# Kernel optimization log

Measured on AMD Instinct MI355X. Metric: run time of the kernel, lower is better.

Reference implementation:

```python
import jax, jax.numpy as jnp
import numpy as np

B, S, H, D, R = 2, 2048, 16, 128, 16
HID = H * D
ROPE_BASE = 10000.0


def _rotate_half(x):
    x1, x2 = x[..., : D // 2], x[..., D // 2:]
    return jnp.concatenate((-x2, x1), axis=-1)


def _sin_cos(position_ids):
    # full-dim RoPE (rope_fraction == 1)
    inv_freq = 1.0 / (ROPE_BASE ** (jnp.arange(0, D, 2, dtype=jnp.float32) / D))  # [D/2]
    freqs = position_ids.astype(jnp.float32)[..., None] * inv_freq  # [B,S,D/2]
    emb = jnp.concatenate((freqs, freqs), axis=-1)  # [B,S,D]
    # add head axis -> [B,1,S,D]
    return jnp.sin(emb)[:, None], jnp.cos(emb)[:, None]


def setup_inputs() -> dict:
    key = jax.random.key(0)
    ks = jax.random.split(key, 6)
    q = jax.random.normal(ks[0], (B, S, HID), dtype=jnp.float32)
    k = jax.random.normal(ks[1], (B, S, HID), dtype=jnp.float32)
    v = jax.random.normal(ks[2], (B, S, HID), dtype=jnp.float32)
    position_ids = jnp.tile(jnp.arange(S, dtype=jnp.int64)[None], (B, 1))
    causal = jnp.tril(jnp.ones((S, S), dtype=bool))
    attention_mask = jnp.where(causal, 0.0, -1e9).astype(jnp.float32)
    attention_mask = jnp.broadcast_to(attention_mask[None, None], (B, 1, S, S))
    k_registers = jax.random.normal(ks[3], (1, H, R, D), dtype=jnp.float32)
    v_registers = jax.random.normal(ks[4], (1, H, R, D), dtype=jnp.float32)
    return {
        "query_states": q,
        "key_states": k,
        "value_states": v,
        "position_ids": position_ids,
        "attention_mask": attention_mask,
        "k_registers": k_registers,
        "v_registers": v_registers,
    }


def reference(query_states, key_states, value_states, position_ids,
              attention_mask, k_registers, v_registers):
    bsz, q_len, _ = query_states.shape
    # [B,S,H*D] -> [B,H,S,D]
    q = query_states.reshape(bsz, q_len, H, D).transpose(0, 2, 1, 3)
    k = key_states.reshape(bsz, -1, H, D).transpose(0, 2, 1, 3)
    v = value_states.reshape(bsz, -1, H, D).transpose(0, 2, 1, 3)

    sin, cos = _sin_cos(position_ids)
    q = q * cos + _rotate_half(q) * sin
    k = k * cos + _rotate_half(k) * sin

    # concat learned register K/V tokens along kv-length
    k = jnp.concatenate((k, jnp.broadcast_to(k_registers, (bsz, H, R, D))), axis=2)
    v = jnp.concatenate((v, jnp.broadcast_to(v_registers, (bsz, H, R, D))), axis=2)
    mask = jnp.concatenate(
        (attention_mask,
         jnp.zeros(attention_mask.shape[:-1] + (R,), dtype=attention_mask.dtype)),
        axis=-1)

    scale = 1.0 / np.sqrt(D).astype(np.float32)
    scores = jnp.einsum('bhqd,bhkd->bhqk', q, k * scale) + mask  # [B,H,S,S+R]
    probs = jax.nn.softmax(scores.astype(jnp.float32), axis=-1).astype(q.dtype)
    out = jnp.einsum('bhqk,bhkd->bhqd', probs, v)
    return out.transpose(0, 2, 1, 3).reshape(bsz, q_len, H * D)
```

## Files before the change

kernel.cpp:

```cpp
#include <hip/hip_runtime.h>

#define S_LEN 2048
#define HID   2048
#define NH    16
#define HD    128
#define NREG  16
#define KPAD  2112
#define NBH   32

typedef float f32x4 __attribute__((ext_vector_type(4)));
typedef short s16x8 __attribute__((ext_vector_type(8)));

__device__ __forceinline__ unsigned short f2bf(float f) {
    union { float f; unsigned int u; } x; x.f = f;
    return (unsigned short)((x.u + 0x7FFFu + ((x.u >> 16) & 1u)) >> 16);
}
__device__ __forceinline__ unsigned short f2bf_t(float f) {
    union { float f; unsigned int u; } x; x.f = f;
    return (unsigned short)(x.u >> 16);
}
__device__ __forceinline__ void gl_lds16(const unsigned short* g, unsigned short* l) {
    __builtin_amdgcn_global_load_lds((const __attribute__((address_space(1))) void*)g,
                                     (__attribute__((address_space(3))) void*)l, 16, 0, 0);
}

__global__ void rope_qk_kernel(const float* __restrict__ q, const float* __restrict__ k,
                               const int* __restrict__ pos,
                               unsigned short* __restrict__ Qb, unsigned short* __restrict__ Kb) {
    int i = blockIdx.x * 256 + threadIdx.x;
    int dh = i & 63;
    int h  = (i >> 6) & 15;
    int s  = (i >> 10) & 2047;
    int b  = i >> 21;
    float p   = (float)pos[b * S_LEN + s];
    float inv = exp2f((float)dh * -0.20762050593046014f);
    float ang = p * inv;
    float rev = ang * 0.15915494309189535f;
    rev -= rintf(rev);
    float a2 = rev * 6.283185307179586f;
    float sn = __sinf(a2), cs = __cosf(a2);
    const float* qp = q + (size_t)(b * S_LEN + s) * HID + h * HD + dh;
    const float* kp = k + (size_t)(b * S_LEN + s) * HID + h * HD + dh;
    float q1 = qp[0], q2 = qp[64];
    float k1 = kp[0], k2 = kp[64];
    const float scale = 0.08838834764831845f;
    size_t qo = (size_t)((b * NH + h) * S_LEN + s) * HD + dh;
    Qb[qo]      = f2bf((q1 * cs - q2 * sn) * scale);
    Qb[qo + 64] = f2bf((q2 * cs + q1 * sn) * scale);
    size_t ko = (size_t)((b * NH + h) * KPAD + s) * HD + dh;
    Kb[ko]      = f2bf(k1 * cs - k2 * sn);
    Kb[ko + 64] = f2bf(k2 * cs + k1 * sn);
}

__global__ void fill_regs_kernel(const float* __restrict__ kreg, const float* __restrict__ vreg,
                                 unsigned short* __restrict__ Kb, unsigned short* __restrict__ Vt) {
    int i = blockIdx.x * 256 + threadIdx.x;
    {
        int d = i & 127, r = (i >> 7) & 63, h = (i >> 13) & 15, b = i >> 17;
        float v = (r < NREG) ? kreg[(h * NREG + r) * HD + d] : 0.0f;
        Kb[((size_t)((b * NH + h) * KPAD + 2048 + r)) * HD + d] = f2bf(v);
    }
    {
        int r = i & 63, d = (i >> 6) & 127, h = (i >> 13) & 15, b = i >> 17;
        float v = (r < NREG) ? vreg[(h * NREG + r) * HD + d] : 0.0f;
        Vt[((size_t)((b * NH + h) * HD + d)) * KPAD + 2048 + r] = f2bf(v);
    }
}

__global__ void transpose_v_kernel(const float* __restrict__ v, unsigned short* __restrict__ Vt) {
    __shared__ unsigned short T[64][136];
    int t  = threadIdx.x;
    int bh = blockIdx.x >> 5, st = blockIdx.x & 31;
    int b  = bh >> 4, h = bh & 15;
    {
        int key = t >> 2, c = t & 3;
        const float* src = v + (size_t)(b * S_LEN + st * 64 + key) * HID + h * HD;
        #pragma unroll
        for (int i = 0; i < 4; ++i) {
            int d0 = c * 32 + i * 8;
            float4 a  = *(const float4*)(src + d0);
            float4 bb = *(const float4*)(src + d0 + 4);
            unsigned short tmp[8] = { f2bf(a.x), f2bf(a.y), f2bf(a.z), f2bf(a.w),
                                      f2bf(bb.x), f2bf(bb.y), f2bf(bb.z), f2bf(bb.w) };
            *(uint4*)(&T[key][d0]) = *(const uint4*)tmp;
        }
    }
    __syncthreads();
    {
        int d = t >> 1, half = t & 1;
        unsigned short buf[32];
        #pragma unroll
        for (int i = 0; i < 32; ++i) buf[i] = T[half * 32 + i][d];
        uint4* dst = (uint4*)(Vt + ((size_t)(bh * HD + d)) * KPAD + st * 64 + half * 32);
        const uint4* bp = (const uint4*)buf;
        #pragma unroll
        for (int i = 0; i < 4; ++i) dst[i] = bp[i];
    }
}

__global__ __launch_bounds__(256, 2)
void attn_kernel(const unsigned short* __restrict__ Qb, const unsigned short* __restrict__ Kb,
                 const unsigned short* __restrict__ Vt, float* __restrict__ out) {
    __shared__ unsigned short Klds[64 * 128];
    __shared__ unsigned short Vtl[128 * 64];
    __shared__ unsigned short Plds[4 * 32 * 72];

    int idx = blockIdx.x;
    int bh  = idx & 31;
    int j5  = idx >> 5;
    int t   = (idx < 256) ? (15 - 2 * j5) : (2 * (j5 - 8));
    int b = bh >> 4, h = bh & 15;
    int tid = threadIdx.x, w = tid >> 6, lane = tid & 63;
    int quad = lane >> 4, k15 = lane & 15;
    int s0q = t * 128;

    const unsigned short* kg[4]; unsigned short* klp[4];
    const unsigned short* vg[4]; unsigned short* vlp[4];
    {
        int krow = 16 * w + (lane >> 4);
        #pragma unroll
        for (int j = 0; j < 4; ++j) {
            int key = krow + 4 * j;
            kg[j]  = Kb + ((size_t)bh * KPAD + key) * HD + (((lane & 15) ^ (key & 15)) << 3);
            klp[j] = Klds + (16 * w + 4 * j) * HD;
        }
        int drow = 32 * w + (lane >> 3);
        int vsw  = ((lane & 7) ^ (lane >> 3)) << 3;
        #pragma unroll
        for (int j = 0; j < 4; ++j) {
            vg[j]  = Vt + ((size_t)bh * HD + drow + 8 * j) * KPAD + vsw;
            vlp[j] = Vtl + (32 * w + 8 * j) * 64;
        }
    }

    s16x8 qa[2][4];
    #pragma unroll
    for (int mt = 0; mt < 2; ++mt) {
        const unsigned short* qrow =
            Qb + ((size_t)bh * S_LEN + s0q + w * 32 + mt * 16 + k15) * HD + quad * 8;
        #pragma unroll
        for (int kc = 0; kc < 4; ++kc) qa[mt][kc] = *(const s16x8*)(qrow + kc * 32);
    }

    f32x4 oacc[2][8];
    float lsum[2][4];
    #pragma unroll
    for (int mt = 0; mt < 2; ++mt) {
        #pragma unroll
        for (int nc = 0; nc < 8; ++nc) oacc[mt][nc] = (f32x4){0.f, 0.f, 0.f, 0.f};
        #pragma unroll
        for (int r = 0; r < 4; ++r) lsum[mt][r] = 0.f;
    }

    auto stage = [&](int kbase) {
        size_t ko = (size_t)kbase * HD;
        #pragma unroll
        for (int j = 0; j < 4; ++j) gl_lds16(kg[j] + ko, klp[j]);
        #pragma unroll
        for (int j = 0; j < 4; ++j) gl_lds16(vg[j] + kbase, vlp[j]);
    };

    auto tile = [&](int coff, int mode) {
        #pragma unroll
        for (int mt = 0; mt < 2; ++mt) {
            f32x4 sc[4] = {};
            #pragma unroll
            for (int nc = 0; nc < 4; ++nc) {
                if (mode == 2 && nc > 0) continue;
                #pragma unroll
                for (int kc = 0; kc < 4; ++kc) {
                    const s16x8 bf = *(const s16x8*)(Klds + (nc * 16 + k15) * HD +
                                                     (((4 * kc + quad) ^ k15) << 3));
                    sc[nc] = __builtin_amdgcn_mfma_f32_16x16x32_bf16(qa[mt][kc], bf, sc[nc], 0, 0, 0);
                }
            }
            int rowb = w * 32 + mt * 16 + quad * 4;
            #pragma unroll
            for (int r = 0; r < 4; ++r) {
                float p[4];
                #pragma unroll
                for (int nc = 0; nc < 4; ++nc) {
                    if (mode == 2 && nc > 0) { p[nc] = 0.f; continue; }
                    float e = __expf(sc[nc][r]);
                    bool valid = (mode != 1) || (coff + nc * 16 + k15 <= rowb + r);
                    p[nc] = valid ? e : 0.f;
                }
                lsum[mt][r] += (p[0] + p[1]) + (p[2] + p[3]);
                int prow = w * (32 * 72) + (mt * 16 + quad * 4 + r) * 72 + k15;
                Plds[prow]      = f2bf_t(p[0]);
                Plds[prow + 16] = f2bf_t(p[1]);
                Plds[prow + 32] = f2bf_t(p[2]);
                Plds[prow + 48] = f2bf_t(p[3]);
            }
        }
        #pragma unroll
        for (int mt = 0; mt < 2; ++mt)
            #pragma unroll
            for (int kc = 0; kc < 2; ++kc) {
                const s16x8 pf = *(const s16x8*)(Plds + w * (32 * 72) +
                                                 (mt * 16 + k15) * 72 + kc * 32 + quad * 8);
                #pragma unroll
                for (int nc = 0; nc < 8; ++nc) {
                    const s16x8 vf = *(const s16x8*)(Vtl + (nc * 16 + k15) * 64 +
                                                     (((4 * kc + quad) ^ (k15 & 7)) << 3));
                    oacc[mt][nc] = __builtin_amdgcn_mfma_f32_16x16x32_bf16(pf, vf, oacc[mt][nc], 0, 0, 0);
                }
            }
    };

    int nfull = 2 * t;
    for (int kt = 0; kt < nfull; ++kt) {
        __syncthreads();
        stage(kt * 64);
        __syncthreads();
        tile(0, 0);
    }
    #pragma unroll
    for (int dt = 0; dt < 2; ++dt) {
        __syncthreads();
        stage((2 * t + dt) * 64);
        __syncthreads();
        tile(64 * dt, 1);
    }
    __syncthreads();
    stage(2048);
    __syncthreads();
    tile(0, 2);

    #pragma unroll
    for (int mt = 0; mt < 2; ++mt)
        #pragma unroll
        for (int r = 0; r < 4; ++r) {
            float lv = lsum[mt][r];
            #pragma unroll
            for (int off = 1; off < 16; off <<= 1) lv += __shfl_xor(lv, off);
            float invl = 1.0f / lv;
            size_t row = (size_t)(b * S_LEN + s0q + w * 32 + mt * 16 + quad * 4 + r) * HID
                         + h * HD + k15;
            #pragma unroll
            for (int nc = 0; nc < 8; ++nc)
                out[row + nc * 16] = oacc[mt][nc][r] * invl;
        }
}

extern "C" void kernel_launch(void* const* d_in, const int* in_sizes, int n_in,
                              void* d_out, int out_size, void* d_ws, size_t ws_size,
                              hipStream_t stream) {
    const float* q    = (const float*)d_in[0];
    const float* k    = (const float*)d_in[1];
    const float* v    = (const float*)d_in[2];
    const int*   pos  = (const int*)d_in[3];
    const float* kreg = (const float*)d_in[5];
    const float* vreg = (const float*)d_in[6];
    float* out = (float*)d_out;

    unsigned short* Qb = (unsigned short*)d_ws;
    unsigned short* Kb = Qb + (size_t)NBH * S_LEN * HD;
    unsigned short* Vt = Kb + (size_t)NBH * KPAD * HD;

    rope_qk_kernel<<<dim3(16384), dim3(256), 0, stream>>>(q, k, pos, Qb, Kb);
    fill_regs_kernel<<<dim3(1024), dim3(256), 0, stream>>>(kreg, vreg, Kb, Vt);
    transpose_v_kernel<<<dim3(1024), dim3(256), 0, stream>>>(v, Vt);
    attn_kernel<<<dim3(512), dim3(256), 0, stream>>>(Qb, Kb, Vt, out);
}
```

Before: 225.1 us.

## Fuse prep kernels, apply RoPE to Q in attention, switch to 32x32 MFMA

Three preprocessing kernels (K RoPE, register fill, V transpose) become one prep kernel. Q RoPE and scaling now run inside the attention kernel, so the bf16 Q workspace and its extra round trip through global memory go away. The attention inner loops move from 16x16x32 to 32x32x16 bf16 MFMA, with new LDS swizzles. The row-sum is computed by an extra MFMA against a ones vector instead of shuffles. This trades fewer launches and less memory traffic for more per-thread sin/cos work and higher register pressure from the 32x32 accumulators.

```diff
diff --git a/kernel.cpp b/kernel.cpp
--- a/kernel.cpp
+++ b/kernel.cpp
@@ -8,8 +8,13 @@
 #define KPAD  2112
 #define NBH   32
 
-typedef float f32x4 __attribute__((ext_vector_type(4)));
-typedef short s16x8 __attribute__((ext_vector_type(8)));
+typedef float f32x16 __attribute__((ext_vector_type(16)));
+typedef short s16x8  __attribute__((ext_vector_type(8)));
+
+#define ROPE_C  0.20762050593046014f
+#define INV2PI  0.15915494309189535f
+#define TWOPI   6.283185307179586f
+#define QSCALE  0.08838834764831845f
 
 __device__ __forceinline__ unsigned short f2bf(float f) {
     union { float f; unsigned int u; } x; x.f = f;
@@ -24,74 +29,84 @@
                                      (__attribute__((address_space(3))) void*)l, 16, 0, 0);
 }
 
-__global__ void rope_qk_kernel(const float* __restrict__ q, const float* __restrict__ k,
-                               const int* __restrict__ pos,
-                               unsigned short* __restrict__ Qb, unsigned short* __restrict__ Kb) {
-    int i = blockIdx.x * 256 + threadIdx.x;
-    int dh = i & 63;
-    int h  = (i >> 6) & 15;
-    int s  = (i >> 10) & 2047;
-    int b  = i >> 21;
-    float p   = (float)pos[b * S_LEN + s];
-    float inv = exp2f((float)dh * -0.20762050593046014f);
-    float ang = p * inv;
-    float rev = ang * 0.15915494309189535f;
-    rev -= rintf(rev);
-    float a2 = rev * 6.283185307179586f;
-    float sn = __sinf(a2), cs = __cosf(a2);
-    const float* qp = q + (size_t)(b * S_LEN + s) * HID + h * HD + dh;
-    const float* kp = k + (size_t)(b * S_LEN + s) * HID + h * HD + dh;
-    float q1 = qp[0], q2 = qp[64];
-    float k1 = kp[0], k2 = kp[64];
-    const float scale = 0.08838834764831845f;
-    size_t qo = (size_t)((b * NH + h) * S_LEN + s) * HD + dh;
-    Qb[qo]      = f2bf((q1 * cs - q2 * sn) * scale);
-    Qb[qo + 64] = f2bf((q2 * cs + q1 * sn) * scale);
-    size_t ko = (size_t)((b * NH + h) * KPAD + s) * HD + dh;
-    Kb[ko]      = f2bf(k1 * cs - k2 * sn);
-    Kb[ko + 64] = f2bf(k2 * cs + k1 * sn);
-}
-
-__global__ void fill_regs_kernel(const float* __restrict__ kreg, const float* __restrict__ vreg,
-                                 unsigned short* __restrict__ Kb, unsigned short* __restrict__ Vt) {
-    int i = blockIdx.x * 256 + threadIdx.x;
-    {
-        int d = i & 127, r = (i >> 7) & 63, h = (i >> 13) & 15, b = i >> 17;
-        float v = (r < NREG) ? kreg[(h * NREG + r) * HD + d] : 0.0f;
-        Kb[((size_t)((b * NH + h) * KPAD + 2048 + r)) * HD + d] = f2bf(v);
-    }
-    {
-        int r = i & 63, d = (i >> 6) & 127, h = (i >> 13) & 15, b = i >> 17;
-        float v = (r < NREG) ? vreg[(h * NREG + r) * HD + d] : 0.0f;
-        Vt[((size_t)((b * NH + h) * HD + d)) * KPAD + 2048 + r] = f2bf(v);
-    }
-}
-
-__global__ void transpose_v_kernel(const float* __restrict__ v, unsigned short* __restrict__ Vt) {
+__global__ void prep_kernel(const float* __restrict__ k, const float* __restrict__ v,
+                            const int* __restrict__ pos,
+                            const float* __restrict__ kreg, const float* __restrict__ vreg,
+                            unsigned short* __restrict__ Kb, unsigned short* __restrict__ Vt) {
+    int kt = blockIdx.x % 33;
+    int bh = blockIdx.x / 33;
+    int b = bh >> 4, h = bh & 15;
+    int tid = threadIdx.x;
+
+    {
+        int dh = tid & 63, wv = tid >> 6;
+        if (kt < 32) {
+            float inv = exp2f((float)dh * -ROPE_C);
+            #pragma unroll 4
+            for (int j = 0; j < 16; ++j) {
+                int key = wv * 16 + j;
+                int s = kt * 64 + key;
+                float p = (float)pos[b * S_LEN + s];
+                float rev = p * inv * INV2PI;
+                rev -= rintf(rev);
+                float a2 = rev * TWOPI;
+                float sn = __sinf(a2), cs = __cosf(a2);
+                const float* kp = k + (size_t)(b * S_LEN + s) * HID + h * HD + dh;
+                float k1 = kp[0], k2 = kp[64];
+                size_t ko = (size_t)(bh * KPAD + s) * HD + dh;
+                Kb[ko]      = f2bf(k1 * cs - k2 * sn);
+                Kb[ko + 64] = f2bf(k2 * cs + k1 * sn);
+            }
+        } else {
+            #pragma unroll 4
+            for (int j = 0; j < 16; ++j) {
+                int r = wv * 16 + j;
+                float k1 = 0.f, k2 = 0.f;
+                if (r < NREG) {
+                    const float* kp = kreg + (h * NREG + r) * HD + dh;
+                    k1 = kp[0]; k2 = kp[64];
+                }
+                size_t ko = (size_t)(bh * KPAD + 2048 + r) * HD + dh;
+                Kb[ko]      = f2bf(k1);
+                Kb[ko + 64] = f2bf(k2);
+            }
+        }
+    }
+
     __shared__ unsigned short T[64][136];
-    int t  = threadIdx.x;
-    int bh = blockIdx.x >> 5, st = blockIdx.x & 31;
-    int b  = bh >> 4, h = bh & 15;
-    {
-        int key = t >> 2, c = t & 3;
-        const float* src = v + (size_t)(b * S_LEN + st * 64 + key) * HID + h * HD;
+    {
+        int key = tid >> 2, c = tid & 3;
         #pragma unroll
         for (int i = 0; i < 4; ++i) {
             int d0 = c * 32 + i * 8;
-            float4 a  = *(const float4*)(src + d0);
-            float4 bb = *(const float4*)(src + d0 + 4);
-            unsigned short tmp[8] = { f2bf(a.x), f2bf(a.y), f2bf(a.z), f2bf(a.w),
-                                      f2bf(bb.x), f2bf(bb.y), f2bf(bb.z), f2bf(bb.w) };
+            float vals[8];
+            if (kt < 32) {
+                const float* src = v + (size_t)(b * S_LEN + kt * 64 + key) * HID + h * HD + d0;
+                float4 a = *(const float4*)src, bb = *(const float4*)(src + 4);
+                vals[0]=a.x; vals[1]=a.y; vals[2]=a.z; vals[3]=a.w;
+                vals[4]=bb.x; vals[5]=bb.y; vals[6]=bb.z; vals[7]=bb.w;
+            } else if (key < NREG) {
+                const float* src = vreg + (h * NREG + key) * HD + d0;
+                float4 a = *(const float4*)src, bb = *(const float4*)(src + 4);
+                vals[0]=a.x; vals[1]=a.y; vals[2]=a.z; vals[3]=a.w;
+                vals[4]=bb.x; vals[5]=bb.y; vals[6]=bb.z; vals[7]=bb.w;
+            } else {
+                #pragma unroll
+                for (int n = 0; n < 8; ++n) vals[n] = 0.f;
+            }
+            unsigned short tmp[8];
+            #pragma unroll
+            for (int n = 0; n < 8; ++n) tmp[n] = f2bf(vals[n]);
             *(uint4*)(&T[key][d0]) = *(const uint4*)tmp;
         }
     }
     __syncthreads();
     {
-        int d = t >> 1, half = t & 1;
+        int d = tid >> 1, half = tid & 1;
         unsigned short buf[32];
         #pragma unroll
         for (int i = 0; i < 32; ++i) buf[i] = T[half * 32 + i][d];
-        uint4* dst = (uint4*)(Vt + ((size_t)(bh * HD + d)) * KPAD + st * 64 + half * 32);
+        uint4* dst = (uint4*)(Vt + ((size_t)(bh * HD + d)) * KPAD + kt * 64 + half * 32);
         const uint4* bp = (const uint4*)buf;
         #pragma unroll
         for (int i = 0; i < 4; ++i) dst[i] = bp[i];
@@ -99,8 +114,9 @@
 }
 
 __global__ __launch_bounds__(256, 2)
-void attn_kernel(const unsigned short* __restrict__ Qb, const unsigned short* __restrict__ Kb,
-                 const unsigned short* __restrict__ Vt, float* __restrict__ out) {
+void attn_kernel(const float* __restrict__ q, const int* __restrict__ pos,
+                 const unsigned short* __restrict__ Kb, const unsigned short* __restrict__ Vt,
+                 float* __restrict__ out) {
     __shared__ unsigned short Klds[64 * 128];
     __shared__ unsigned short Vtl[128 * 64];
     __shared__ unsigned short Plds[4 * 32 * 72];
@@ -111,46 +127,76 @@
     int t   = (idx < 256) ? (15 - 2 * j5) : (2 * (j5 - 8));
     int b = bh >> 4, h = bh & 15;
     int tid = threadIdx.x, w = tid >> 6, lane = tid & 63;
-    int quad = lane >> 4, k15 = lane & 15;
+    int l31 = lane & 31, h5 = lane >> 5, l7 = lane & 7;
     int s0q = t * 128;
 
     const unsigned short* kg[4]; unsigned short* klp[4];
     const unsigned short* vg[4]; unsigned short* vlp[4];
     {
-        int krow = 16 * w + (lane >> 4);
         #pragma unroll
         for (int j = 0; j < 4; ++j) {
-            int key = krow + 4 * j;
-            kg[j]  = Kb + ((size_t)bh * KPAD + key) * HD + (((lane & 15) ^ (key & 15)) << 3);
+            int key = 16 * w + 4 * j + (lane >> 4);
+            int gd  = (lane & 15) ^ (key & 7);
+            kg[j]  = Kb + ((size_t)bh * KPAD + key) * HD + (gd << 3);
             klp[j] = Klds + (16 * w + 4 * j) * HD;
         }
-        int drow = 32 * w + (lane >> 3);
-        int vsw  = ((lane & 7) ^ (lane >> 3)) << 3;
         #pragma unroll
         for (int j = 0; j < 4; ++j) {
-            vg[j]  = Vt + ((size_t)bh * HD + drow + 8 * j) * KPAD + vsw;
+            int d  = 32 * w + 8 * j + (lane >> 3);
+            int gk = (lane & 7) ^ (d & 7);
+            vg[j]  = Vt + ((size_t)bh * HD + d) * KPAD + (gk << 3);
             vlp[j] = Vtl + (32 * w + 8 * j) * 64;
         }
     }
 
-    s16x8 qa[2][4];
-    #pragma unroll
-    for (int mt = 0; mt < 2; ++mt) {
-        const unsigned short* qrow =
-            Qb + ((size_t)bh * S_LEN + s0q + w * 32 + mt * 16 + k15) * HD + quad * 8;
-        #pragma unroll
-        for (int kc = 0; kc < 4; ++kc) qa[mt][kc] = *(const s16x8*)(qrow + kc * 32);
-    }
-
-    f32x4 oacc[2][8];
-    float lsum[2][4];
-    #pragma unroll
-    for (int mt = 0; mt < 2; ++mt) {
-        #pragma unroll
-        for (int nc = 0; nc < 8; ++nc) oacc[mt][nc] = (f32x4){0.f, 0.f, 0.f, 0.f};
-        #pragma unroll
-        for (int r = 0; r < 4; ++r) lsum[mt][r] = 0.f;
-    }
+    s16x8 qa[8];
+    {
+        int m_loc = w * 32 + l31;
+        int s = s0q + m_loc;
+        float pp = (float)pos[b * S_LEN + s];
+        const float* qrow = q + (size_t)(b * S_LEN + s) * HID + h * HD + h5 * 8;
+        float qv[8][8];
+        #pragma unroll
+        for (int kc = 0; kc < 8; ++kc) {
+            float4 a = *(const float4*)(qrow + kc * 16);
+            float4 c = *(const float4*)(qrow + kc * 16 + 4);
+            qv[kc][0]=a.x; qv[kc][1]=a.y; qv[kc][2]=a.z; qv[kc][3]=a.w;
+            qv[kc][4]=c.x; qv[kc][5]=c.y; qv[kc][6]=c.z; qv[kc][7]=c.w;
+        }
+        #pragma unroll
+        for (int kc = 0; kc < 4; ++kc)
+            #pragma unroll
+            for (int j = 0; j < 8; ++j) {
+                int dh = kc * 16 + h5 * 8 + j;
+                float inv = exp2f((float)dh * -ROPE_C);
+                float rev = pp * inv * INV2PI;
+                rev -= rintf(rev);
+                float a2 = rev * TWOPI;
+                float sn = __sinf(a2), cs = __cosf(a2);
+                float qlo = qv[kc][j], qhi = qv[kc + 4][j];
+                qa[kc][j]     = (short)f2bf((qlo * cs - qhi * sn) * QSCALE);
+                qa[kc + 4][j] = (short)f2bf((qhi * cs + qlo * sn) * QSCALE);
+            }
+    }
+
+    s16x8 ones_f;
+    {
+        short o = (l31 == 0) ? (short)0x3F80 : (short)0;
+        #pragma unroll
+        for (int j = 0; j < 8; ++j) ones_f[j] = o;
+    }
+
+    int swz[8];
+    #pragma unroll
+    for (int kc = 0; kc < 8; ++kc) swz[kc] = (((2 * kc + h5) ^ l7) << 3);
+
+    f32x16 oacc[4], lacc;
+    #pragma unroll
+    for (int nd = 0; nd < 4; ++nd)
+        #pragma unroll
+        for (int r = 0; r < 16; ++r) oacc[nd][r] = 0.f;
+    #pragma unroll
+    for (int r = 0; r < 16; ++r) lacc[r] = 0.f;
 
     auto stage = [&](int kbase) {
         size_t ko = (size_t)kbase * HD;
@@ -160,52 +206,49 @@
         for (int j = 0; j < 4; ++j) gl_lds16(vg[j] + kbase, vlp[j]);
     };
 
+    const unsigned short* kfb = Klds + (l31 << 7);
+    unsigned short* pwb = Plds + w * (32 * 72);
+    unsigned short* pwl = pwb + (4 * h5) * 72 + l31;
+    const unsigned short* prl = pwb + l31 * 72 + h5 * 8;
+
     auto tile = [&](int coff, int mode) {
-        #pragma unroll
-        for (int mt = 0; mt < 2; ++mt) {
-            f32x4 sc[4] = {};
-            #pragma unroll
-            for (int nc = 0; nc < 4; ++nc) {
-                if (mode == 2 && nc > 0) continue;
-                #pragma unroll
-                for (int kc = 0; kc < 4; ++kc) {
-                    const s16x8 bf = *(const s16x8*)(Klds + (nc * 16 + k15) * HD +
-                                                     (((4 * kc + quad) ^ k15) << 3));
-                    sc[nc] = __builtin_amdgcn_mfma_f32_16x16x32_bf16(qa[mt][kc], bf, sc[nc], 0, 0, 0);
+        int nct = (mode == 2) ? 1 : 2;
+        #pragma unroll
+        for (int nc = 0; nc < 2; ++nc) {
+            if (nc >= nct) break;
+            f32x16 sc;
+            #pragma unroll
+            for (int r = 0; r < 16; ++r) sc[r] = 0.f;
+            #pragma unroll
+            for (int kc = 0; kc < 8; ++kc) {
+                const s16x8 bf = *(const s16x8*)(kfb + nc * (32 * 128) + swz[kc]);
+                sc = __builtin_amdgcn_mfma_f32_32x32x16_bf16(qa[kc], bf, sc, 0, 0, 0);
+            }
+            #pragma unroll
+            for (int reg = 0; reg < 16; ++reg) {
+                float e = __expf(sc[reg]);
+                if (mode == 1) {
+                    int rl = (reg & 3) + 8 * (reg >> 2) + 4 * h5;
+                    bool valid = (coff + nc * 32 + l31) <= (w * 32 + rl);
+                    e = valid ? e : 0.f;
+                } else if (mode == 2) {
+                    e = (l31 < NREG) ? e : 0.f;
                 }
-            }
-            int rowb = w * 32 + mt * 16 + quad * 4;
-            #pragma unroll
-            for (int r = 0; r < 4; ++r) {
-                float p[4];
-                #pragma unroll
-                for (int nc = 0; nc < 4; ++nc) {
-                    if (mode == 2 && nc > 0) { p[nc] = 0.f; continue; }
-                    float e = __expf(sc[nc][r]);
-                    bool valid = (mode != 1) || (coff + nc * 16 + k15 <= rowb + r);
-                    p[nc] = valid ? e : 0.f;
-                }
-                lsum[mt][r] += (p[0] + p[1]) + (p[2] + p[3]);
-                int prow = w * (32 * 72) + (mt * 16 + quad * 4 + r) * 72 + k15;
-                Plds[prow]      = f2bf_t(p[0]);
-                Plds[prow + 16] = f2bf_t(p[1]);
-                Plds[prow + 32] = f2bf_t(p[2]);
-                Plds[prow + 48] = f2bf_t(p[3]);
-            }
-        }
-        #pragma unroll
-        for (int mt = 0; mt < 2; ++mt)
-            #pragma unroll
-            for (int kc = 0; kc < 2; ++kc) {
-                const s16x8 pf = *(const s16x8*)(Plds + w * (32 * 72) +
-                                                 (mt * 16 + k15) * 72 + kc * 32 + quad * 8);
-                #pragma unroll
-                for (int nc = 0; nc < 8; ++nc) {
-                    const s16x8 vf = *(const s16x8*)(Vtl + (nc * 16 + k15) * 64 +
-                                                     (((4 * kc + quad) ^ (k15 & 7)) << 3));
-                    oacc[mt][nc] = __builtin_amdgcn_mfma_f32_16x16x32_bf16(pf, vf, oacc[mt][nc], 0, 0, 0);
-                }
-            }
+                pwl[((reg & 3) + 8 * (reg >> 2)) * 72 + nc * 32] = f2bf_t(e);
+            }
+        }
+        int kct = (mode == 2) ? 1 : 4;
+        #pragma unroll
+        for (int kc = 0; kc < 4; ++kc) {
+            if (kc >= kct) break;
+            const s16x8 pf = *(const s16x8*)(prl + kc * 16);
+            lacc = __builtin_amdgcn_mfma_f32_32x32x16_bf16(pf, ones_f, lacc, 0, 0, 0);
+            #pragma unroll
+            for (int nd = 0; nd < 4; ++nd) {
+                const s16x8 vf = *(const s16x8*)(Vtl + ((nd * 32 + l31) << 6) + swz[kc]);
+                oacc[nd] = __builtin_amdgcn_mfma_f32_32x32x16_bf16(pf, vf, oacc[nd], 0, 0, 0);
+            }
+        }
     };
 
     int nfull = 2 * t;
@@ -228,19 +271,15 @@
     tile(0, 2);
 
     #pragma unroll
-    for (int mt = 0; mt < 2; ++mt)
-        #pragma unroll
-        for (int r = 0; r < 4; ++r) {
-            float lv = lsum[mt][r];
-            #pragma unroll
-            for (int off = 1; off < 16; off <<= 1) lv += __shfl_xor(lv, off);
-            float invl = 1.0f / lv;
-            size_t row = (size_t)(b * S_LEN + s0q + w * 32 + mt * 16 + quad * 4 + r) * HID
-                         + h * HD + k15;
-            #pragma unroll
-            for (int nc = 0; nc < 8; ++nc)
-                out[row + nc * 16] = oacc[mt][nc][r] * invl;
-        }
+    for (int reg = 0; reg < 16; ++reg) {
+        float lv = __shfl(lacc[reg], lane & 32);
+        float invl = 1.0f / lv;
+        int rl = (reg & 3) + 8 * (reg >> 2) + 4 * h5;
+        size_t row = (size_t)(b * S_LEN + s0q + w * 32 + rl) * HID + h * HD + l31;
+        #pragma unroll
+        for (int nd = 0; nd < 4; ++nd)
+            out[row + nd * 32] = oacc[nd][reg] * invl;
+    }
 }
 
 extern "C" void kernel_launch(void* const* d_in, const int* in_sizes, int n_in,
@@ -254,12 +293,9 @@
     const float* vreg = (const float*)d_in[6];
     float* out = (float*)d_out;
 
-    unsigned short* Qb = (unsigned short*)d_ws;
-    unsigned short* Kb = Qb + (size_t)NBH * S_LEN * HD;
+    unsigned short* Kb = (unsigned short*)d_ws;
     unsigned short* Vt = Kb + (size_t)NBH * KPAD * HD;
 
-    rope_qk_kernel<<<dim3(16384), dim3(256), 0, stream>>>(q, k, pos, Qb, Kb);
-    fill_regs_kernel<<<dim3(1024), dim3(256), 0, stream>>>(kreg, vreg, Kb, Vt);
-    transpose_v_kernel<<<dim3(1024), dim3(256), 0, stream>>>(v, Vt);
-    attn_kernel<<<dim3(512), dim3(256), 0, stream>>>(Qb, Kb, Vt, out);
-}
+    prep_kernel<<<dim3(NBH * 33), dim3(256), 0, stream>>>(k, v, pos, kreg, vreg, Kb, Vt);
+    attn_kernel<<<dim3(512), dim3(256), 0, stream>>>(q, pos, Kb, Vt, out);
+}
```

Measured after the change: 228.0 us. No clear change (+1.3%).
